# Kernel tuning notes

Hardware: AMD Instinct MI355X
Metric: run time of the kernel (lower is better)

## Reference

```python
import jax, jax.numpy as jnp
import numpy as np

NX, NZ = 256, 256   # grid size
NT = 400            # time steps
NS = 4              # shots (batched wavefields)
NR = 128            # receivers
DX = DZ = 10.0      # grid spacing (m)
DT = 1.0e-3         # time step (s)
F0 = 10.0           # dominant frequency (Hz)
NABC = 30           # absorbing boundary width (cells)


def setup_inputs() -> dict:
    key = jax.random.key(0)
    k1, k2, k3, k4 = jax.random.split(key, 4)
    # velocity 1500-4000 m/s, density 1000-2000 kg/m^3
    vp = 1500.0 + 2500.0 * jax.random.uniform(k1, (NX, NZ), dtype=jnp.float32)
    rho = 1000.0 + 1000.0 * jax.random.uniform(k2, (NX, NZ), dtype=jnp.float32)
    # PML-style quadratic damping profile (bc_pml analogue)
    ix = np.arange(NX, dtype=np.float64)
    iz = np.arange(NZ, dtype=np.float64)
    dist_x = np.maximum(np.maximum(NABC - ix, ix - (NX - 1 - NABC)), 0.0) / NABC
    dist_z = np.maximum(np.maximum(NABC - iz, iz - (NZ - 1 - NABC)), 0.0) / NABC
    d0 = 3.0 * 4000.0 * np.log(1000.0) / (2.0 * NABC * DX)
    damp = jnp.asarray(d0 * (dist_x[:, None] ** 2 + dist_z[None, :] ** 2), dtype=jnp.float32)
    # Ricker wavelet, one trace per shot
    t = np.arange(NT) * DT - 1.2 / F0
    a = (np.pi * F0 * t) ** 2
    wav = ((1.0 - 2.0 * a) * np.exp(-a)).astype(np.float32)
    wavelet = jnp.tile(jnp.asarray(wav)[None, :], (NS, 1))
    src_x = jax.random.randint(k3, (NS,), NABC + 2, NX - NABC - 2)
    src_z = jnp.full((NS,), NABC + 2, dtype=jnp.int32)
    rcv_x = jnp.sort(jax.random.randint(k4, (NR,), NABC + 2, NX - NABC - 2))
    rcv_z = jnp.full((NR,), NABC + 2, dtype=jnp.int32)
    return dict(vp=vp, rho=rho, damp=damp, wavelet=wavelet,
                src_x=src_x, src_z=src_z, rcv_x=rcv_x, rcv_z=rcv_z)


# staggered-grid first-order differences (zero-padded at boundary)
def _dxf(a):
    return jnp.pad(a[:, 1:, :] - a[:, :-1, :], ((0, 0), (0, 1), (0, 0)))

def _dxb(a):
    return jnp.pad(a[:, 1:, :] - a[:, :-1, :], ((0, 0), (1, 0), (0, 0)))

def _dzf(a):
    return jnp.pad(a[:, :, 1:] - a[:, :, :-1], ((0, 0), (0, 0), (0, 1)))

def _dzb(a):
    return jnp.pad(a[:, :, 1:] - a[:, :, :-1], ((0, 0), (0, 0), (1, 0)))


def reference(vp, rho, damp, wavelet, src_x, src_z, rcv_x, rcv_z):
    """Stress-velocity acoustic FD propagator with absorbing damping.
    Returns recorded pressure at receivers: [src_n, nt, rcv_n]."""
    ns = wavelet.shape[0]
    nx, nz = vp.shape
    kappa = rho * vp * vp          # bulk modulus [nx, nz]
    fac = 1.0 - DT * damp          # damping factor [nx, nz]
    binv = DT / rho                # buoyancy * dt
    shot = jnp.arange(ns)
    src_amp = DT / (DX * DZ)

    def step(carry, wav_t):
        p, vx, vz = carry
        vx = fac * vx - binv * _dxf(p) / DX
        vz = fac * vz - binv * _dzf(p) / DZ
        p = fac * p - DT * kappa * (_dxb(vx) / DX + _dzb(vz) / DZ)
        p = p.at[shot, src_x, src_z].add(wav_t * src_amp)
        rec = p[:, rcv_x, rcv_z]   # [ns, nr]
        return (p, vx, vz), rec

    zero = jnp.zeros((ns, nx, nz), vp.dtype)
    _, recs = jax.lax.scan(step, (zero, zero, zero), wavelet.T)  # [nt, ns, nr]
    return jnp.transpose(recs, (1, 0, 2))
```

## Files before the change

kernel.cpp:

```cpp
#include <hip/hip_runtime.h>


#define NXc 256
#define NZc 256
#define NTc 400
#define NSc 4
#define NRc 128

#define TS 16
#define Bt 32
#define LROW 64
#define ROWS 64
#define NSTR 16
#define BT 1024
#define LSZ ((ROWS + 2) * LROW)
#define NBLK (NSc * 64)
#define NEP (NTc / TS)

constexpr float DT_H    = 0.001f;
constexpr float INV_D   = 0.1f;
constexpr float SRC_AMP = 0.001f * 0.01f;
constexpr int   NXZ     = NXc * NZc;

typedef float f32x4 __attribute__((ext_vector_type(4)));

__device__ __forceinline__ unsigned ldu_far(const unsigned* p) {
    unsigned v;
    asm volatile("global_load_dword %0, %1, off sc0 sc1\n\t"
                 "s_waitcnt vmcnt(0)" : "=&v"(v) : "v"(p) : "memory");
    return v;
}
__device__ __forceinline__ void stu_far(unsigned* p, unsigned v) {
    asm volatile("global_store_dword %0, %1, off sc0 sc1"
                 :: "v"(p), "v"(v) : "memory");
}

__global__ __launch_bounds__(BT) void prop_kernel(
    float* __restrict__ xchg, unsigned* __restrict__ flags,
    const float* __restrict__ vp, const float* __restrict__ rho,
    const float* __restrict__ damp, const float* __restrict__ wavelet,
    const int* __restrict__ src_x, const int* __restrict__ src_z,
    const int* __restrict__ rcv_x, const int* __restrict__ rcv_z,
    float* __restrict__ out)
{
    __shared__ float sp[LSZ], svx[LSZ];

    const int tid  = threadIdx.x;
    const int bid  = blockIdx.x;
    const int s    = bid >> 6;
    const int tile = bid & 63;
    const int tx = tile >> 3, tz = tile & 7;
    const int gx0 = tx * Bt - TS, gz0 = tz * Bt - TS;

    const int li  = tid >> 4;
    const int st  = tid & 15;
    const int lk0 = st * 4;
    const int gi  = gx0 + li;
    const int gk0 = gz0 + lk0;
    const bool in = ((unsigned)gi < (unsigned)NXc) &&
                    ((unsigned)gk0 < (unsigned)NZc);
    const int c4 = s * NXZ + gi * NZc + gk0;
    const bool central = in && ((unsigned)(li - TS) < (unsigned)Bt)
                            && (lk0 >= TS) && (lk0 <= TS + Bt - 4);
    const bool ring = in && !central;

    const size_t F = (size_t)NSc * NXZ;
    float* b0 = xchg;
    float* b1 = xchg + 3 * F;

    float pr[4]  = {0, 0, 0, 0};
    float vxr[4] = {0, 0, 0, 0};
    float vzr[4] = {0, 0, 0, 0};
    float fr[4], bxr[4], bzr[4], dkxr[4], dkzr[4], sfr[4];
    {
        const int sx = src_x[s], sz = src_z[s];
        if (in) {
            float4 r4 = *(const float4*)(rho  + c4 - s * NXZ);
            float4 v4 = *(const float4*)(vp   + c4 - s * NXZ);
            float4 d4 = *(const float4*)(damp + c4 - s * NXZ);
            float rv[4] = {r4.x, r4.y, r4.z, r4.w};
            float vv[4] = {v4.x, v4.y, v4.z, v4.w};
            float dv[4] = {d4.x, d4.y, d4.z, d4.w};
#pragma unroll
            for (int k = 0; k < 4; ++k) {
                int gk = gk0 + k;
                fr[k] = 1.0f - DT_H * dv[k];
                float bi = DT_H / rv[k] * INV_D;
                bxr[k] = (gi == NXc - 1) ? 0.f : bi;
                bzr[k] = (gk == NZc - 1) ? 0.f : bi;
                float dk = DT_H * rv[k] * vv[k] * vv[k] * INV_D;
                dkxr[k] = (gi == 0) ? 0.f : dk;
                dkzr[k] = (gk == 0) ? 0.f : dk;
                sfr[k]  = (gi == sx && gk == sz) ? SRC_AMP : 0.f;
            }
        } else {
#pragma unroll
            for (int k = 0; k < 4; ++k) {
                fr[k] = 0.f; bxr[k] = 0.f; bzr[k] = 0.f;
                dkxr[k] = 0.f; dkzr[k] = 0.f; sfr[k] = 0.f;
            }
        }
    }

    if (tid < LROW) {
        sp[tid] = 0.f; svx[tid] = 0.f;
        sp[LSZ - LROW + tid] = 0.f; svx[LSZ - LROW + tid] = 0.f;
    }

    int rxv = 0, rzv = 0;
    if (tid < NRc) { rxv = rcv_x[tid]; rzv = rcv_z[tid]; }
    const bool rown = (tid < NRc) &&
        ((unsigned)(rxv - tx * Bt) < (unsigned)Bt) &&
        ((unsigned)(rzv - tz * Bt) < (unsigned)Bt);
    const int rj = (rxv - gx0 + 1) * LROW + (rzv - gz0);
    float* obase = out + (size_t)s * NTc * NRc + tid;
    const float* wb = wavelet + s * NTc;

    int nbid = -1;
    if (tid < 9 && tid != 4) {
        int dx = tid / 3 - 1, dz = tid - (tid / 3) * 3 - 1;
        int nx2 = tx + dx, nz2 = tz + dz;
        if (((unsigned)nx2 < 8u) && ((unsigned)nz2 < 8u))
            nbid = (s << 6) + nx2 * 8 + nz2;
    }

    const int jb = (li + 1) * LROW + lk0;

    *(float4*)&sp[jb] = make_float4(pr[0], pr[1], pr[2], pr[3]);

    for (int l = 0; l < NEP; ++l) {
        const bool notLast = (l < NEP - 1);
        float* pb = (l & 1) ? b1 : b0;
        __syncthreads();

        for (int tau = 0; tau < TS; ++tau) {
            float4 pn4 = *(const float4*)&sp[jb + LROW];
            float  pze = __shfl_down(pr[0], 1, 64);
            float pnx[4] = {pn4.x, pn4.y, pn4.z, pn4.w};
            float pz1[4] = {pr[1], pr[2], pr[3], pze};
#pragma unroll
            for (int k = 0; k < 4; ++k) {
                vxr[k] = fr[k] * vxr[k] - bxr[k] * (pnx[k] - pr[k]);
                vzr[k] = fr[k] * vzr[k] - bzr[k] * (pz1[k] - pr[k]);
            }
            *(float4*)&svx[jb] = make_float4(vxr[0], vxr[1], vxr[2], vxr[3]);
            __syncthreads();

            const float wv = wb[l * TS + tau];
            float4 vxm4 = *(const float4*)&svx[jb - LROW];
            float  vzm0 = __shfl_up(vzr[3], 1, 64);
            float vxm[4] = {vxm4.x, vxm4.y, vxm4.z, vxm4.w};
            float vzm[4] = {vzm0, vzr[0], vzr[1], vzr[2]};
#pragma unroll
            for (int k = 0; k < 4; ++k) {
                pr[k] = fr[k] * pr[k]
                      - dkxr[k] * (vxr[k] - vxm[k])
                      - dkzr[k] * (vzr[k] - vzm[k])
                      + sfr[k] * wv;
            }
            if (tau == TS - 1 && notLast && central) {
                f32x4 a = {pr[0], pr[1], pr[2], pr[3]};
                f32x4 b = {vxr[0], vxr[1], vxr[2], vxr[3]};
                f32x4 c = {vzr[0], vzr[1], vzr[2], vzr[3]};
                asm volatile(
                    "global_store_dwordx4 %0, %3, off sc0 sc1\n\t"
                    "global_store_dwordx4 %1, %4, off sc0 sc1\n\t"
                    "global_store_dwordx4 %2, %5, off sc0 sc1"
                    :: "v"(pb + c4), "v"(pb + F + c4), "v"(pb + 2 * F + c4),
                       "v"(a), "v"(b), "v"(c)
                    : "memory");
            }
            *(float4*)&sp[jb] = make_float4(pr[0], pr[1], pr[2], pr[3]);
            __syncthreads();

            if (tau < TS - 1 && rown)
                obase[(size_t)(l * TS + tau) * NRc] = sp[rj];
        }

        if (notLast) {
            asm volatile("s_waitcnt vmcnt(0)" ::: "memory");
            __syncthreads();
            if (tid == 0) stu_far(flags + bid, (unsigned)(l + 1));
            if (rown) obase[(size_t)(l * TS + TS - 1) * NRc] = sp[rj];
            if (nbid >= 0) {
                const unsigned want = (unsigned)(l + 1);
                const unsigned* fp = flags + nbid;
                while (ldu_far(fp) < want) __builtin_amdgcn_s_sleep(2);
            }
            __syncthreads();
            if (ring) {
                f32x4 a, b, c;
                asm volatile(
                    "global_load_dwordx4 %0, %3, off sc0 sc1\n\t"
                    "global_load_dwordx4 %1, %4, off sc0 sc1\n\t"
                    "global_load_dwordx4 %2, %5, off sc0 sc1\n\t"
                    "s_waitcnt vmcnt(0)"
                    : "=&v"(a), "=&v"(b), "=&v"(c)
                    : "v"(pb + c4), "v"(pb + F + c4), "v"(pb + 2 * F + c4)
                    : "memory");
                pr[0]=a.x; pr[1]=a.y; pr[2]=a.z; pr[3]=a.w;
                vxr[0]=b.x; vxr[1]=b.y; vxr[2]=b.z; vxr[3]=b.w;
                vzr[0]=c.x; vzr[1]=c.y; vzr[2]=c.z; vzr[3]=c.w;
                *(float4*)&sp[jb] = make_float4(pr[0], pr[1], pr[2], pr[3]);
            }
        } else {
            if (rown) obase[(size_t)(l * TS + TS - 1) * NRc] = sp[rj];
        }
    }
}

extern "C" void kernel_launch(void* const* d_in, const int* in_sizes, int n_in,
                              void* d_out, int out_size, void* d_ws, size_t ws_size,
                              hipStream_t stream)
{
    const float* vp      = (const float*)d_in[0];
    const float* rho     = (const float*)d_in[1];
    const float* damp    = (const float*)d_in[2];
    const float* wavelet = (const float*)d_in[3];
    const int*   src_x   = (const int*)d_in[4];
    const int*   src_z   = (const int*)d_in[5];
    const int*   rcv_x   = (const int*)d_in[6];
    const int*   rcv_z   = (const int*)d_in[7];
    float* out = (float*)d_out;
    float* ws  = (float*)d_ws;

    const size_t F = (size_t)NSc * NXZ;
    float* xchg = ws;
    unsigned* flags = (unsigned*)(ws + 6 * F);

    hipMemsetAsync(flags, 0, NBLK * sizeof(unsigned), stream);

    prop_kernel<<<NBLK, BT, 0, stream>>>(
        xchg, flags, vp, rho, damp, wavelet,
        src_x, src_z, rcv_x, rcv_z, out);
}
```

Before: 327.0 us.

## Process two x-rows per thread with half the threads per block

Each thread now owns two adjacent x-rows of 4 z-points, so the block runs 512 threads instead of 1024. The x-derivative between the two rows stays in registers, and only odd-row vx goes through shared memory, which roughly halves LDS traffic and per-step work per thread. The cost is more registers per thread and fewer waves to hide the latency of the per-step barriers.

After: 375.1 us. 14.7% more time.

```diff
diff --git a/kernel.cpp b/kernel.cpp
--- a/kernel.cpp
+++ b/kernel.cpp
@@ -11,9 +11,11 @@
 #define Bt 32
 #define LROW 64
 #define ROWS 64
+#define TR 32
 #define NSTR 16
-#define BT 1024
-#define LSZ ((ROWS + 2) * LROW)
+#define BT 512
+#define SPSZ ((ROWS + 2) * LROW)
+#define SVSZ ((TR + 1) * LROW)
 #define NBLK (NSc * 64)
 #define NEP (NTc / TS)
 
@@ -43,7 +45,8 @@
     const int* __restrict__ rcv_x, const int* __restrict__ rcv_z,
     float* __restrict__ out)
 {
-    __shared__ float sp[LSZ], svx[LSZ];
+    __shared__ float sp[SPSZ];
+    __shared__ float svo[SVSZ];
 
     const int tid  = threadIdx.x;
     const int bid  = blockIdx.x;
@@ -52,60 +55,72 @@
     const int tx = tile >> 3, tz = tile & 7;
     const int gx0 = tx * Bt - TS, gz0 = tz * Bt - TS;
 
-    const int li  = tid >> 4;
+    const int li2 = tid >> 4;
     const int st  = tid & 15;
     const int lk0 = st * 4;
-    const int gi  = gx0 + li;
+    const int gi0 = gx0 + 2 * li2;
     const int gk0 = gz0 + lk0;
-    const bool in = ((unsigned)gi < (unsigned)NXc) &&
+    const bool in = ((unsigned)gi0 < (unsigned)NXc) &&
                     ((unsigned)gk0 < (unsigned)NZc);
-    const int c4 = s * NXZ + gi * NZc + gk0;
-    const bool central = in && ((unsigned)(li - TS) < (unsigned)Bt)
-                            && (lk0 >= TS) && (lk0 <= TS + Bt - 4);
+    const int c40 = s * NXZ + gi0 * NZc + gk0;
+    const bool central = in && ((unsigned)(li2 - 8) < 16u)
+                            && (st >= 4) && (st < 12);
     const bool ring = in && !central;
 
     const size_t F = (size_t)NSc * NXZ;
     float* b0 = xchg;
     float* b1 = xchg + 3 * F;
 
-    float pr[4]  = {0, 0, 0, 0};
-    float vxr[4] = {0, 0, 0, 0};
-    float vzr[4] = {0, 0, 0, 0};
-    float fr[4], bxr[4], bzr[4], dkxr[4], dkzr[4], sfr[4];
+    float pr[2][4]  = {{0,0,0,0},{0,0,0,0}};
+    float vxr[2][4] = {{0,0,0,0},{0,0,0,0}};
+    float vzr[2][4] = {{0,0,0,0},{0,0,0,0}};
+    float fr[2][4], bxr[2][4], bzr[2][4], dkxr[2][4], dkzr[2][4], sfr[2][4];
     {
         const int sx = src_x[s], sz = src_z[s];
-        if (in) {
-            float4 r4 = *(const float4*)(rho  + c4 - s * NXZ);
-            float4 v4 = *(const float4*)(vp   + c4 - s * NXZ);
-            float4 d4 = *(const float4*)(damp + c4 - s * NXZ);
-            float rv[4] = {r4.x, r4.y, r4.z, r4.w};
-            float vv[4] = {v4.x, v4.y, v4.z, v4.w};
-            float dv[4] = {d4.x, d4.y, d4.z, d4.w};
-#pragma unroll
-            for (int k = 0; k < 4; ++k) {
-                int gk = gk0 + k;
-                fr[k] = 1.0f - DT_H * dv[k];
-                float bi = DT_H / rv[k] * INV_D;
-                bxr[k] = (gi == NXc - 1) ? 0.f : bi;
-                bzr[k] = (gk == NZc - 1) ? 0.f : bi;
-                float dk = DT_H * rv[k] * vv[k] * vv[k] * INV_D;
-                dkxr[k] = (gi == 0) ? 0.f : dk;
-                dkzr[k] = (gk == 0) ? 0.f : dk;
-                sfr[k]  = (gi == sx && gk == sz) ? SRC_AMP : 0.f;
-            }
-        } else {
-#pragma unroll
-            for (int k = 0; k < 4; ++k) {
-                fr[k] = 0.f; bxr[k] = 0.f; bzr[k] = 0.f;
-                dkxr[k] = 0.f; dkzr[k] = 0.f; sfr[k] = 0.f;
+#pragma unroll
+        for (int r = 0; r < 2; ++r) {
+            const int gi = gi0 + r;
+            if (in) {
+                const int g = gi * NZc + gk0;
+                float4 r4 = *(const float4*)(rho  + g);
+                float4 v4 = *(const float4*)(vp   + g);
+                float4 d4 = *(const float4*)(damp + g);
+                float rv[4] = {r4.x, r4.y, r4.z, r4.w};
+                float vv[4] = {v4.x, v4.y, v4.z, v4.w};
+                float dv[4] = {d4.x, d4.y, d4.z, d4.w};
+#pragma unroll
+                for (int k = 0; k < 4; ++k) {
+                    int gk = gk0 + k;
+                    fr[r][k] = 1.0f - DT_H * dv[k];
+                    float bi = DT_H / rv[k] * INV_D;
+                    bxr[r][k] = (gi == NXc - 1) ? 0.f : bi;
+                    bzr[r][k] = (gk == NZc - 1) ? 0.f : bi;
+                    float dk = DT_H * rv[k] * vv[k] * vv[k] * INV_D;
+                    dkxr[r][k] = (gi == 0) ? 0.f : dk;
+                    dkzr[r][k] = (gk == 0) ? 0.f : dk;
+                    sfr[r][k]  = (gi == sx && gk == sz) ? SRC_AMP : 0.f;
+                }
+            } else {
+#pragma unroll
+                for (int k = 0; k < 4; ++k) {
+                    fr[r][k]=0.f; bxr[r][k]=0.f; bzr[r][k]=0.f;
+                    dkxr[r][k]=0.f; dkzr[r][k]=0.f; sfr[r][k]=0.f;
+                }
             }
         }
     }
 
+    const int jp0 = (2 * li2 + 1) * LROW + lk0;
+    const int jvo = (li2 + 1) * LROW + lk0;
+
     if (tid < LROW) {
-        sp[tid] = 0.f; svx[tid] = 0.f;
-        sp[LSZ - LROW + tid] = 0.f; svx[LSZ - LROW + tid] = 0.f;
-    }
+        sp[tid] = 0.f;
+        sp[SPSZ - LROW + tid] = 0.f;
+        svo[tid] = 0.f;
+    }
+    *(f32x4*)&sp[jp0] = f32x4{0,0,0,0};
+    *(f32x4*)&sp[jp0 + LROW] = f32x4{0,0,0,0};
+    *(f32x4*)&svo[jvo] = f32x4{0,0,0,0};
 
     int rxv = 0, rzv = 0;
     if (tid < NRc) { rxv = rcv_x[tid]; rzv = rcv_z[tid]; }
@@ -124,53 +139,77 @@
             nbid = (s << 6) + nx2 * 8 + nz2;
     }
 
-    const int jb = (li + 1) * LROW + lk0;
-
-    *(float4*)&sp[jb] = make_float4(pr[0], pr[1], pr[2], pr[3]);
-
     for (int l = 0; l < NEP; ++l) {
         const bool notLast = (l < NEP - 1);
         float* pb = (l & 1) ? b1 : b0;
         __syncthreads();
 
         for (int tau = 0; tau < TS; ++tau) {
-            float4 pn4 = *(const float4*)&sp[jb + LROW];
-            float  pze = __shfl_down(pr[0], 1, 64);
-            float pnx[4] = {pn4.x, pn4.y, pn4.z, pn4.w};
-            float pz1[4] = {pr[1], pr[2], pr[3], pze};
-#pragma unroll
-            for (int k = 0; k < 4; ++k) {
-                vxr[k] = fr[k] * vxr[k] - bxr[k] * (pnx[k] - pr[k]);
-                vzr[k] = fr[k] * vzr[k] - bzr[k] * (pz1[k] - pr[k]);
-            }
-            *(float4*)&svx[jb] = make_float4(vxr[0], vxr[1], vxr[2], vxr[3]);
+            f32x4 pn = *(const f32x4*)&sp[jp0 + 2 * LROW];
+            float pze0 = __shfl_down(pr[0][0], 1, 64);
+            float pze1 = __shfl_down(pr[1][0], 1, 64);
+            {
+                float pz1a[4] = {pr[0][1], pr[0][2], pr[0][3], pze0};
+                float pz1b[4] = {pr[1][1], pr[1][2], pr[1][3], pze1};
+#pragma unroll
+                for (int k = 0; k < 4; ++k) {
+                    vxr[0][k] = fr[0][k]*vxr[0][k]
+                              - bxr[0][k]*(pr[1][k] - pr[0][k]);
+                    vzr[0][k] = fr[0][k]*vzr[0][k]
+                              - bzr[0][k]*(pz1a[k] - pr[0][k]);
+                    vxr[1][k] = fr[1][k]*vxr[1][k]
+                              - bxr[1][k]*(pn[k] - pr[1][k]);
+                    vzr[1][k] = fr[1][k]*vzr[1][k]
+                              - bzr[1][k]*(pz1b[k] - pr[1][k]);
+                }
+            }
+            *(f32x4*)&svo[jvo] =
+                f32x4{vxr[1][0], vxr[1][1], vxr[1][2], vxr[1][3]};
             __syncthreads();
 
             const float wv = wb[l * TS + tau];
-            float4 vxm4 = *(const float4*)&svx[jb - LROW];
-            float  vzm0 = __shfl_up(vzr[3], 1, 64);
-            float vxm[4] = {vxm4.x, vxm4.y, vxm4.z, vxm4.w};
-            float vzm[4] = {vzm0, vzr[0], vzr[1], vzr[2]};
-#pragma unroll
-            for (int k = 0; k < 4; ++k) {
-                pr[k] = fr[k] * pr[k]
-                      - dkxr[k] * (vxr[k] - vxm[k])
-                      - dkzr[k] * (vzr[k] - vzm[k])
-                      + sfr[k] * wv;
+            f32x4 vxm = *(const f32x4*)&svo[jvo - LROW];
+            float vzm0 = __shfl_up(vzr[0][3], 1, 64);
+            float vzm1 = __shfl_up(vzr[1][3], 1, 64);
+            {
+                float vza[4] = {vzm0, vzr[0][0], vzr[0][1], vzr[0][2]};
+                float vzb[4] = {vzm1, vzr[1][0], vzr[1][1], vzr[1][2]};
+#pragma unroll
+                for (int k = 0; k < 4; ++k) {
+                    pr[0][k] = fr[0][k]*pr[0][k]
+                             - dkxr[0][k]*(vxr[0][k] - vxm[k])
+                             - dkzr[0][k]*(vzr[0][k] - vza[k])
+                             + sfr[0][k]*wv;
+                    pr[1][k] = fr[1][k]*pr[1][k]
+                             - dkxr[1][k]*(vxr[1][k] - vxr[0][k])
+                             - dkzr[1][k]*(vzr[1][k] - vzb[k])
+                             + sfr[1][k]*wv;
+                }
             }
             if (tau == TS - 1 && notLast && central) {
-                f32x4 a = {pr[0], pr[1], pr[2], pr[3]};
-                f32x4 b = {vxr[0], vxr[1], vxr[2], vxr[3]};
-                f32x4 c = {vzr[0], vzr[1], vzr[2], vzr[3]};
+                f32x4 pa = {pr[0][0], pr[0][1], pr[0][2], pr[0][3]};
+                f32x4 pc = {pr[1][0], pr[1][1], pr[1][2], pr[1][3]};
+                f32x4 xa = {vxr[0][0], vxr[0][1], vxr[0][2], vxr[0][3]};
+                f32x4 xc = {vxr[1][0], vxr[1][1], vxr[1][2], vxr[1][3]};
+                f32x4 za = {vzr[0][0], vzr[0][1], vzr[0][2], vzr[0][3]};
+                f32x4 zc = {vzr[1][0], vzr[1][1], vzr[1][2], vzr[1][3]};
                 asm volatile(
-                    "global_store_dwordx4 %0, %3, off sc0 sc1\n\t"
-                    "global_store_dwordx4 %1, %4, off sc0 sc1\n\t"
-                    "global_store_dwordx4 %2, %5, off sc0 sc1"
-                    :: "v"(pb + c4), "v"(pb + F + c4), "v"(pb + 2 * F + c4),
-                       "v"(a), "v"(b), "v"(c)
+                    "global_store_dwordx4 %0, %6, off sc0 sc1\n\t"
+                    "global_store_dwordx4 %1, %7, off sc0 sc1\n\t"
+                    "global_store_dwordx4 %2, %8, off sc0 sc1\n\t"
+                    "global_store_dwordx4 %3, %9, off sc0 sc1\n\t"
+                    "global_store_dwordx4 %4, %10, off sc0 sc1\n\t"
+                    "global_store_dwordx4 %5, %11, off sc0 sc1"
+                    :: "v"(pb + c40), "v"(pb + c40 + NZc),
+                       "v"(pb + F + c40), "v"(pb + F + c40 + NZc),
+                       "v"(pb + 2*F + c40), "v"(pb + 2*F + c40 + NZc),
+                       "v"(pa), "v"(pc), "v"(xa), "v"(xc), "v"(za), "v"(zc)
                     : "memory");
             }
-            *(float4*)&sp[jb] = make_float4(pr[0], pr[1], pr[2], pr[3]);
+            *(f32x4*)&sp[jp0] =
+                f32x4{pr[0][0], pr[0][1], pr[0][2], pr[0][3]};
+            *(f32x4*)&sp[jp0 + LROW] =
+                f32x4{pr[1][0], pr[1][1], pr[1][2], pr[1][3]};
             __syncthreads();
 
             if (tau < TS - 1 && rown)
@@ -189,19 +228,30 @@
             }
             __syncthreads();
             if (ring) {
-                f32x4 a, b, c;
+                f32x4 pa, pc, xa, xc, za, zc;
                 asm volatile(
-                    "global_load_dwordx4 %0, %3, off sc0 sc1\n\t"
-                    "global_load_dwordx4 %1, %4, off sc0 sc1\n\t"
-                    "global_load_dwordx4 %2, %5, off sc0 sc1\n\t"
+                    "global_load_dwordx4 %0, %6, off sc0 sc1\n\t"
+                    "global_load_dwordx4 %1, %7, off sc0 sc1\n\t"
+                    "global_load_dwordx4 %2, %8, off sc0 sc1\n\t"
+                    "global_load_dwordx4 %3, %9, off sc0 sc1\n\t"
+                    "global_load_dwordx4 %4, %10, off sc0 sc1\n\t"
+                    "global_load_dwordx4 %5, %11, off sc0 sc1\n\t"
                     "s_waitcnt vmcnt(0)"
-                    : "=&v"(a), "=&v"(b), "=&v"(c)
-                    : "v"(pb + c4), "v"(pb + F + c4), "v"(pb + 2 * F + c4)
+                    : "=&v"(pa), "=&v"(pc), "=&v"(xa), "=&v"(xc),
+                      "=&v"(za), "=&v"(zc)
+                    : "v"(pb + c40), "v"(pb + c40 + NZc),
+                      "v"(pb + F + c40), "v"(pb + F + c40 + NZc),
+                      "v"(pb + 2*F + c40), "v"(pb + 2*F + c40 + NZc)
                     : "memory");
-                pr[0]=a.x; pr[1]=a.y; pr[2]=a.z; pr[3]=a.w;
-                vxr[0]=b.x; vxr[1]=b.y; vxr[2]=b.z; vxr[3]=b.w;
-                vzr[0]=c.x; vzr[1]=c.y; vzr[2]=c.z; vzr[3]=c.w;
-                *(float4*)&sp[jb] = make_float4(pr[0], pr[1], pr[2], pr[3]);
+#pragma unroll
+                for (int k = 0; k < 4; ++k) {
+                    pr[0][k] = pa[k];  pr[1][k] = pc[k];
+                    vxr[0][k] = xa[k]; vxr[1][k] = xc[k];
+                    vzr[0][k] = za[k]; vzr[1][k] = zc[k];
+                }
+                *(f32x4*)&sp[jp0] = pa;
+                *(f32x4*)&sp[jp0 + LROW] = pc;
+                *(f32x4*)&svo[jvo] = xc;
             }
         } else {
             if (rown) obase[(size_t)(l * TS + TS - 1) * NRc] = sp[rj];
```

## Recompute neighbor velocities redundantly to halve barriers per time step

Applied to the files above, without the earlier changes.

Each thread now also updates the velocity of its x-minus and z-minus neighbours in registers, reading both p rows from a double-buffered shared pressure array. The shared velocity exchange and one of the two barriers per time step go away. Pressure is ping-ponged between two shared buffers so each step needs only one barrier after its write. The cost is redundant velocity arithmetic, extra coefficient registers and an extra shared load per step.

Result: faster. 286.0 us (-12.5%).

```diff
diff --git a/kernel.cpp b/kernel.cpp
--- a/kernel.cpp
+++ b/kernel.cpp
@@ -11,9 +11,8 @@
 #define Bt 32
 #define LROW 64
 #define ROWS 64
-#define NSTR 16
 #define BT 1024
-#define LSZ ((ROWS + 2) * LROW)
+#define SPSZ ((ROWS + 2) * LROW)
 #define NBLK (NSc * 64)
 #define NEP (NTc / TS)
 
@@ -43,7 +42,7 @@
     const int* __restrict__ rcv_x, const int* __restrict__ rcv_z,
     float* __restrict__ out)
 {
-    __shared__ float sp[LSZ], svx[LSZ];
+    __shared__ float sp[2 * SPSZ];
 
     const int tid  = threadIdx.x;
     const int bid  = blockIdx.x;
@@ -71,13 +70,18 @@
     float pr[4]  = {0, 0, 0, 0};
     float vxr[4] = {0, 0, 0, 0};
     float vzr[4] = {0, 0, 0, 0};
+    float vxm[4] = {0, 0, 0, 0};
+    float vzm    = 0.f;
     float fr[4], bxr[4], bzr[4], dkxr[4], dkzr[4], sfr[4];
+    float fxm[4], bxm[4];
+    float fzm = 0.f, bzm = 0.f;
     {
         const int sx = src_x[s], sz = src_z[s];
         if (in) {
-            float4 r4 = *(const float4*)(rho  + c4 - s * NXZ);
-            float4 v4 = *(const float4*)(vp   + c4 - s * NXZ);
-            float4 d4 = *(const float4*)(damp + c4 - s * NXZ);
+            const int g = gi * NZc + gk0;
+            float4 r4 = *(const float4*)(rho  + g);
+            float4 v4 = *(const float4*)(vp   + g);
+            float4 d4 = *(const float4*)(damp + g);
             float rv[4] = {r4.x, r4.y, r4.z, r4.w};
             float vv[4] = {v4.x, v4.y, v4.z, v4.w};
             float dv[4] = {d4.x, d4.y, d4.z, d4.w};
@@ -93,18 +97,39 @@
                 dkzr[k] = (gk == 0) ? 0.f : dk;
                 sfr[k]  = (gi == sx && gk == sz) ? SRC_AMP : 0.f;
             }
+            if (gi > 0) {
+                float4 rm = *(const float4*)(rho  + g - NZc);
+                float4 dm = *(const float4*)(damp + g - NZc);
+                float rmv[4] = {rm.x, rm.y, rm.z, rm.w};
+                float dmv[4] = {dm.x, dm.y, dm.z, dm.w};
+#pragma unroll
+                for (int k = 0; k < 4; ++k) {
+                    fxm[k] = 1.0f - DT_H * dmv[k];
+                    bxm[k] = DT_H / rmv[k] * INV_D;
+                }
+            } else {
+#pragma unroll
+                for (int k = 0; k < 4; ++k) { fxm[k] = 0.f; bxm[k] = 0.f; }
+            }
+            if (gk0 > 0) {
+                fzm = 1.0f - DT_H * damp[g - 1];
+                bzm = DT_H / rho[g - 1] * INV_D;
+            }
         } else {
 #pragma unroll
             for (int k = 0; k < 4; ++k) {
-                fr[k] = 0.f; bxr[k] = 0.f; bzr[k] = 0.f;
-                dkxr[k] = 0.f; dkzr[k] = 0.f; sfr[k] = 0.f;
-            }
-        }
-    }
+                fr[k]=0.f; bxr[k]=0.f; bzr[k]=0.f;
+                dkxr[k]=0.f; dkzr[k]=0.f; sfr[k]=0.f;
+                fxm[k]=0.f; bxm[k]=0.f;
+            }
+        }
+    }
+
+    const int jp = (li + 1) * LROW + lk0;
 
     if (tid < LROW) {
-        sp[tid] = 0.f; svx[tid] = 0.f;
-        sp[LSZ - LROW + tid] = 0.f; svx[LSZ - LROW + tid] = 0.f;
+        sp[tid] = 0.f;               sp[SPSZ - LROW + tid] = 0.f;
+        sp[SPSZ + tid] = 0.f;        sp[2 * SPSZ - LROW + tid] = 0.f;
     }
 
     int rxv = 0, rzv = 0;
@@ -124,64 +149,75 @@
             nbid = (s << 6) + nx2 * 8 + nz2;
     }
 
-    const int jb = (li + 1) * LROW + lk0;
-
-    *(float4*)&sp[jb] = make_float4(pr[0], pr[1], pr[2], pr[3]);
+    auto STEP = [&](int rdo, int wro, int t, bool pub, float* pb) {
+        f32x4 pn = *(const f32x4*)&sp[rdo + jp + LROW];
+        f32x4 pm = *(const f32x4*)&sp[rdo + jp - LROW];
+        float pze = __shfl_down(pr[0], 1, 64);
+        float pmz = __shfl_up(pr[3], 1, 64);
+        float pz1[4] = {pr[1], pr[2], pr[3], pze};
+#pragma unroll
+        for (int k = 0; k < 4; ++k) {
+            vxr[k] = fr[k] * vxr[k] - bxr[k] * (pn[k]  - pr[k]);
+            vzr[k] = fr[k] * vzr[k] - bzr[k] * (pz1[k] - pr[k]);
+        }
+#pragma unroll
+        for (int k = 0; k < 4; ++k)
+            vxm[k] = fxm[k] * vxm[k] - bxm[k] * (pr[k] - pm[k]);
+        vzm = fzm * vzm - bzm * (pr[0] - pmz);
+        const float wv = wb[t];
+        pr[0] = fr[0]*pr[0] - dkxr[0]*(vxr[0]-vxm[0])
+              - dkzr[0]*(vzr[0]-vzm) + sfr[0]*wv;
+#pragma unroll
+        for (int k = 1; k < 4; ++k)
+            pr[k] = fr[k]*pr[k] - dkxr[k]*(vxr[k]-vxm[k])
+                  - dkzr[k]*(vzr[k]-vzr[k-1]) + sfr[k]*wv;
+        if (pub) {
+            f32x4 a = {pr[0], pr[1], pr[2], pr[3]};
+            f32x4 b = {vxr[0], vxr[1], vxr[2], vxr[3]};
+            f32x4 c = {vzr[0], vzr[1], vzr[2], vzr[3]};
+            asm volatile(
+                "global_store_dwordx4 %0, %3, off sc0 sc1\n\t"
+                "global_store_dwordx4 %1, %4, off sc0 sc1\n\t"
+                "global_store_dwordx4 %2, %5, off sc0 sc1"
+                :: "v"(pb + c4), "v"(pb + F + c4), "v"(pb + 2 * F + c4),
+                   "v"(a), "v"(b), "v"(c)
+                : "memory");
+        }
+        *(f32x4*)&sp[wro + jp] = f32x4{pr[0], pr[1], pr[2], pr[3]};
+        __syncthreads();
+    };
 
     for (int l = 0; l < NEP; ++l) {
         const bool notLast = (l < NEP - 1);
         float* pb = (l & 1) ? b1 : b0;
+
+        *(f32x4*)&sp[jp]        = f32x4{pr[0], pr[1], pr[2], pr[3]};
+        *(f32x4*)&sp[SPSZ + jp] = f32x4{vxr[0], vxr[1], vxr[2], vxr[3]};
         __syncthreads();
-
-        for (int tau = 0; tau < TS; ++tau) {
-            float4 pn4 = *(const float4*)&sp[jb + LROW];
-            float  pze = __shfl_down(pr[0], 1, 64);
-            float pnx[4] = {pn4.x, pn4.y, pn4.z, pn4.w};
-            float pz1[4] = {pr[1], pr[2], pr[3], pze};
-#pragma unroll
-            for (int k = 0; k < 4; ++k) {
-                vxr[k] = fr[k] * vxr[k] - bxr[k] * (pnx[k] - pr[k]);
-                vzr[k] = fr[k] * vzr[k] - bzr[k] * (pz1[k] - pr[k]);
-            }
-            *(float4*)&svx[jb] = make_float4(vxr[0], vxr[1], vxr[2], vxr[3]);
-            __syncthreads();
-
-            const float wv = wb[l * TS + tau];
-            float4 vxm4 = *(const float4*)&svx[jb - LROW];
-            float  vzm0 = __shfl_up(vzr[3], 1, 64);
-            float vxm[4] = {vxm4.x, vxm4.y, vxm4.z, vxm4.w};
-            float vzm[4] = {vzm0, vzr[0], vzr[1], vzr[2]};
-#pragma unroll
-            for (int k = 0; k < 4; ++k) {
-                pr[k] = fr[k] * pr[k]
-                      - dkxr[k] * (vxr[k] - vxm[k])
-                      - dkzr[k] * (vzr[k] - vzm[k])
-                      + sfr[k] * wv;
-            }
-            if (tau == TS - 1 && notLast && central) {
-                f32x4 a = {pr[0], pr[1], pr[2], pr[3]};
-                f32x4 b = {vxr[0], vxr[1], vxr[2], vxr[3]};
-                f32x4 c = {vzr[0], vzr[1], vzr[2], vzr[3]};
-                asm volatile(
-                    "global_store_dwordx4 %0, %3, off sc0 sc1\n\t"
-                    "global_store_dwordx4 %1, %4, off sc0 sc1\n\t"
-                    "global_store_dwordx4 %2, %5, off sc0 sc1"
-                    :: "v"(pb + c4), "v"(pb + F + c4), "v"(pb + 2 * F + c4),
-                       "v"(a), "v"(b), "v"(c)
-                    : "memory");
-            }
-            *(float4*)&sp[jb] = make_float4(pr[0], pr[1], pr[2], pr[3]);
-            __syncthreads();
-
-            if (tau < TS - 1 && rown)
-                obase[(size_t)(l * TS + tau) * NRc] = sp[rj];
+        {
+            f32x4 vm = *(const f32x4*)&sp[SPSZ + jp - LROW];
+            vxm[0]=vm[0]; vxm[1]=vm[1]; vxm[2]=vm[2]; vxm[3]=vm[3];
+            vzm = __shfl_up(vzr[3], 1, 64);
+        }
+        __syncthreads();
+
+        const int tb = l * TS;
+        for (int t2 = 0; t2 < TS; t2 += 2) {
+            STEP(0, SPSZ, tb + t2, false, pb);
+            if (tid < NRc && rown)
+                obase[(size_t)(tb + t2) * NRc] = sp[SPSZ + rj];
+            const bool lastT = (t2 + 2 == TS);
+            STEP(SPSZ, 0, tb + t2 + 1,
+                 lastT && notLast && central, pb);
+            if (!lastT && rown)
+                obase[(size_t)(tb + t2 + 1) * NRc] = sp[rj];
         }
 
         if (notLast) {
             asm volatile("s_waitcnt vmcnt(0)" ::: "memory");
             __syncthreads();
             if (tid == 0) stu_far(flags + bid, (unsigned)(l + 1));
-            if (rown) obase[(size_t)(l * TS + TS - 1) * NRc] = sp[rj];
+            if (rown) obase[(size_t)(tb + TS - 1) * NRc] = sp[rj];
             if (nbid >= 0) {
                 const unsigned want = (unsigned)(l + 1);
                 const unsigned* fp = flags + nbid;
@@ -201,10 +237,9 @@
                 pr[0]=a.x; pr[1]=a.y; pr[2]=a.z; pr[3]=a.w;
                 vxr[0]=b.x; vxr[1]=b.y; vxr[2]=b.z; vxr[3]=b.w;
                 vzr[0]=c.x; vzr[1]=c.y; vzr[2]=c.z; vzr[3]=c.w;
-                *(float4*)&sp[jb] = make_float4(pr[0], pr[1], pr[2], pr[3]);
             }
         } else {
-            if (rown) obase[(size_t)(l * TS + TS - 1) * NRc] = sp[rj];
+            if (rown) obase[(size_t)(tb + TS - 1) * NRc] = sp[rj];
         }
     }
 }
```
